# Kernel tuning notes

Measured on AMD Instinct MI355X. Metric: run time of the kernel, lower is better.

Reference implementation:

```python
import jax, jax.numpy as jnp
from jax import lax
import numpy as np

NPOINT, K, EPS = 2048, 16, 1e-5


def fps(xyz, npoint):
    # Farthest point sampling. Deterministic start index 0 (torch uses randint).
    B, N, _ = xyz.shape
    def step(carry, _):
        distance, far = carry
        centroid = jnp.take_along_axis(xyz, far[:, None, None], axis=1)  # [B,1,3]
        d = jnp.sum((xyz - centroid) ** 2, axis=-1)                      # [B,N]
        distance = jnp.minimum(distance, d)
        return (distance, jnp.argmax(distance, axis=-1)), far
    init = (jnp.full((B, N), 1e10, dtype=xyz.dtype), jnp.zeros((B,), jnp.int32))
    _, cent = lax.scan(step, init, None, length=npoint)  # [npoint, B]
    return jnp.transpose(cent)  # [B, npoint]


def gather(points, idx):
    # points [B,N,C], idx [B,...] -> [B,...,C]
    return jax.vmap(lambda p, i: p[i])(points, idx)


def bn_relu(x, gamma, beta):
    # x [B,S,K,C]; BatchNorm2d training-mode stats over (B,S,K) per channel
    mu = jnp.mean(x, axis=(0, 1, 2), keepdims=True)
    var = jnp.var(x, axis=(0, 1, 2), keepdims=True)
    return jax.nn.relu((x - mu) * lax.rsqrt(var + EPS) * gamma + beta)


def setup_inputs() -> dict:
    key = jax.random.key(0)
    ks = jax.random.split(key, 8)
    B, N, C_in, C_out = 4, 8192, 64, 128
    return {
        'xyz': jax.random.normal(ks[0], (B, N, 3), jnp.float32),
        'feat': jax.random.normal(ks[1], (B, N, C_in), jnp.float32),
        'W1': jax.random.normal(ks[2], (C_in + 3, C_out), jnp.float32) * 0.05,
        'g1': jnp.ones((C_out,), jnp.float32),
        'b1': jnp.zeros((C_out,), jnp.float32),
        'W2': jax.random.normal(ks[3], (C_out, C_out), jnp.float32) * 0.05,
        'g2': jnp.ones((C_out,), jnp.float32),
        'b2': jnp.zeros((C_out,), jnp.float32),
    }


def reference(xyz, feat, W1, g1, b1, W2, g2, b2):
    fps_idx = fps(xyz, NPOINT)
    new_xyz = gather(xyz, fps_idx)                              # [B,S,3]
    # squared distances [B,S,N] via ||a||^2 + ||b||^2 - 2 a.b (avoids [B,S,N,3])
    d = (jnp.sum(new_xyz ** 2, -1)[:, :, None]
         + jnp.sum(xyz ** 2, -1)[:, None, :]
         - 2.0 * jnp.einsum('bsc,bnc->bsn', new_xyz, xyz))
    _, idx = lax.top_k(-d, K)                                   # [B,S,K] smallest dists
    g_xyz = gather(xyz, idx)                                    # [B,S,K,3]
    g_feat = gather(feat, idx)                                  # [B,S,K,C]
    x = jnp.concatenate([g_feat, g_xyz - new_xyz[:, :, None]], axis=-1)
    x = bn_relu(jnp.einsum('bskc,co->bsko', x, W1), g1, b1)     # 1x1 conv == matmul
    x = bn_relu(jnp.einsum('bskc,co->bsko', x, W2), g2, b2)
    new_feat = jnp.max(x, axis=2)                               # max over K -> [B,S,Cout]
    return new_xyz, new_feat
```

## Files before the change

kernel.cpp:

```cpp
#include <hip/hip_runtime.h>
#include <hip/hip_bf16.h>

#define N_PTS 8192
#define N_SAMP 2048
#define KNN_K 16
#define NBATCH 4
#define BN_M (NBATCH * N_SAMP * KNN_K)
#define NROWS (N_SAMP * NBATCH * KNN_K)

typedef float f32x2 __attribute__((ext_vector_type(2)));

template <int CTRL, int RM>
__device__ __forceinline__ unsigned umax_dpp(unsigned v) {
  unsigned o = (unsigned)__builtin_amdgcn_update_dpp((int)v, (int)v, CTRL, RM, 0xF, false);
  return (o > v) ? o : v;
}

__global__ __launch_bounds__(512) void fps_kernel(const float* __restrict__ xyz,
                                                  int* __restrict__ fps_idx,
                                                  float* __restrict__ new_xyz) {
#pragma clang fp contract(off)
  __shared__ __align__(16) float xyzw[N_PTS * 4];
  __shared__ int samp[N_SAMP];
  __shared__ unsigned redbuf[8];
  __shared__ unsigned winslot[2];
  const int b = blockIdx.x;
  const int tid = threadIdx.x;
  const int lane = tid & 63;
  const int wid = tid >> 6;
  const float* base = xyz + (size_t)b * N_PTS * 3;
  for (int i = tid; i < N_PTS * 3; i += 512) {
    float v = base[i];
    int p = i / 3, c = i - p * 3;
    xyzw[p * 4 + c] = v;
  }
  for (int i = tid; i < N_PTS; i += 512) xyzw[i * 4 + 3] = 0.f;
  if (tid == 0) { winslot[0] = 0u; winslot[1] = 0xFFFFFFFFu; }
  __syncthreads();

  f32x2 px[8], py[8], pz[8], dmin[8];
#pragma unroll
  for (int j = 0; j < 8; ++j) {
    int p0 = (2 * j) * 512 + tid, p1 = p0 + 512;
    const float4 a = *reinterpret_cast<const float4*>(&xyzw[p0 * 4]);
    const float4 c = *reinterpret_cast<const float4*>(&xyzw[p1 * 4]);
    px[j] = f32x2{a.x, c.x};
    py[j] = f32x2{a.y, c.y};
    pz[j] = f32x2{a.z, c.z};
    dmin[j] = f32x2{1e10f, 1e10f};
  }
  for (int it = 1; it < N_SAMP; ++it) {
    const int p = it & 1;
    const unsigned cur = winslot[p ^ 1];
    if (tid == 0) samp[it - 1] = (int)cur;
    const float4 c4 = *reinterpret_cast<const float4*>(&xyzw[cur * 4]);
    f32x2 cX = {c4.x, c4.x}, cY = {c4.y, c4.y}, cZ = {c4.z, c4.z};
#pragma unroll
    for (int j = 0; j < 8; ++j) {
      f32x2 dx = px[j] - cX;
      f32x2 dy = py[j] - cY;
      f32x2 dz = pz[j] - cZ;
      f32x2 s01 = dx * dx + dy * dy;
      f32x2 d = s01 + dz * dz;
      dmin[j].x = fminf(dmin[j].x, d.x);
      dmin[j].y = fminf(dmin[j].y, d.y);
    }
    f32x2 m0 = {fmaxf(dmin[0].x, dmin[1].x), fmaxf(dmin[0].y, dmin[1].y)};
    f32x2 m1 = {fmaxf(dmin[2].x, dmin[3].x), fmaxf(dmin[2].y, dmin[3].y)};
    f32x2 m2 = {fmaxf(dmin[4].x, dmin[5].x), fmaxf(dmin[4].y, dmin[5].y)};
    f32x2 m3 = {fmaxf(dmin[6].x, dmin[7].x), fmaxf(dmin[6].y, dmin[7].y)};
    f32x2 n0 = {fmaxf(m0.x, m1.x), fmaxf(m0.y, m1.y)};
    f32x2 n1 = {fmaxf(m2.x, m3.x), fmaxf(m2.y, m3.y)};
    f32x2 nn = {fmaxf(n0.x, n1.x), fmaxf(n0.y, n1.y)};
    const unsigned bd = __float_as_uint(fmaxf(nn.x, nn.y));
    unsigned r = bd;
    r = umax_dpp<0xB1, 0xF>(r);
    r = umax_dpp<0x4E, 0xF>(r);
    r = umax_dpp<0x124, 0xF>(r);
    r = umax_dpp<0x128, 0xF>(r);
    r = umax_dpp<0x142, 0xA>(r);
    r = umax_dpp<0x143, 0xC>(r);
    if (lane == 63) redbuf[wid] = r;
    __syncthreads();
    if (tid == 0) winslot[p ^ 1] = 0xFFFFFFFFu;
    unsigned g = redbuf[lane & 7];
    g = umax_dpp<0xB1, 0xF>(g);
    g = umax_dpp<0x4E, 0xF>(g);
    g = umax_dpp<0x124, 0xF>(g);
    if (bd == g) {
      unsigned cand = 0xFFFFFFFFu;
#pragma unroll
      for (int j = 7; j >= 0; --j) {
        if (__float_as_uint(dmin[j].y) == g) cand = (unsigned)((2 * j + 1) * 512 + tid);
        if (__float_as_uint(dmin[j].x) == g) cand = (unsigned)((2 * j) * 512 + tid);
      }
      atomicMin(&winslot[p], cand);
    }
    __syncthreads();
  }
  if (tid == 0) samp[N_SAMP - 1] = (int)winslot[(N_SAMP - 1) & 1];
  __syncthreads();
  for (int s = tid; s < N_SAMP; s += 512) {
    int idx = samp[s];
    fps_idx[b * N_SAMP + s] = idx;
    size_t o = ((size_t)b * N_SAMP + s) * 3;
    new_xyz[o] = xyzw[idx * 4 + 0];
    new_xyz[o + 1] = xyzw[idx * 4 + 1];
    new_xyz[o + 2] = xyzw[idx * 4 + 2];
  }
}

__global__ __launch_bounds__(256) void knn_kernel(const float* __restrict__ xyz,
                                                  const float* __restrict__ new_xyz,
                                                  int* __restrict__ knn_idx) {
  const int wid = threadIdx.x >> 6, lane = threadIdx.x & 63;
  const int q = blockIdx.x * 4 + wid;
  const int b = q >> 11;
  const float* qp = new_xyz + (size_t)q * 3;
  float q0 = qp[0], q1 = qp[1], q2 = qp[2];
  float qn = __fadd_rn(__fadd_rn(__fmul_rn(q0, q0), __fmul_rn(q1, q1)), __fmul_rn(q2, q2));
  const float* pb = xyz + (size_t)b * N_PTS * 3;
  unsigned long long arr[16];
#pragma unroll
  for (int i = 0; i < 16; ++i) arr[i] = ~0ull;
  for (int p = lane; p < N_PTS; p += 64) {
    float p0 = pb[p * 3 + 0], p1 = pb[p * 3 + 1], p2 = pb[p * 3 + 2];
    float pn = __fadd_rn(__fadd_rn(__fmul_rn(p0, p0), __fmul_rn(p1, p1)), __fmul_rn(p2, p2));
    float dt = fmaf(q2, p2, fmaf(q1, p1, __fmul_rn(q0, p0)));
    float d = __fsub_rn(__fadd_rn(qn, pn), __fmul_rn(2.0f, dt));
    unsigned ub = __float_as_uint(d);
    ub ^= (unsigned)((int)ub >> 31) | 0x80000000u;
    unsigned long long key = ((unsigned long long)ub << 32) | (unsigned)p;
    if (key < arr[15]) {
      unsigned long long curk = key;
#pragma unroll
      for (int j = 0; j < 16; ++j) {
        unsigned long long lo = (curk < arr[j]) ? curk : arr[j];
        unsigned long long hi = (curk < arr[j]) ? arr[j] : curk;
        arr[j] = lo; curk = hi;
      }
    }
  }
  for (int r = 0; r < KNN_K; ++r) {
    unsigned long long m = arr[0];
#pragma unroll
    for (int o = 32; o > 0; o >>= 1) {
      unsigned long long other = __shfl_xor(m, o, 64);
      m = (other < m) ? other : m;
    }
    if (arr[0] == m) {
#pragma unroll
      for (int j = 0; j < 15; ++j) arr[j] = arr[j + 1];
      arr[15] = ~0ull;
    }
    if (lane == r) knn_idx[(size_t)q * KNN_K + r] = (int)(m & 0xFFFFFFFFu);
  }
}

__global__ __launch_bounds__(256) void gemm1_kernel(
    const float* __restrict__ xyz, const float* __restrict__ feat,
    const float* __restrict__ W1, const float* __restrict__ new_xyz,
    const int* __restrict__ knn_i, float* __restrict__ y1, float* __restrict__ stats1) {
  __shared__ __align__(16) float At[67 * 128];
  __shared__ __align__(16) float Wq[17 * 128];
  __shared__ float part[4 * 256];
  __shared__ int nb[128];
  const int t = threadIdx.x, blk = blockIdx.x;
  const int row0 = blk * 128;
  if (t < 128) nb[t] = knn_i[row0 + t];
  __syncthreads();
  {
    const int r = t >> 1, q = t & 1;
    const int rg = row0 + r, bs = rg >> 4, b = bs >> 11;
    const float* fr = feat + ((size_t)b * N_PTS + nb[r]) * 64 + q * 32;
#pragma unroll
    for (int i = 0; i < 8; ++i) {
      float4 v = *reinterpret_cast<const float4*>(fr + 4 * i);
      int c = q * 32 + 4 * i;
      At[(c + 0) * 128 + r] = v.x; At[(c + 1) * 128 + r] = v.y;
      At[(c + 2) * 128 + r] = v.z; At[(c + 3) * 128 + r] = v.w;
    }
    if (q == 0) {
      const float* pr = xyz + ((size_t)b * N_PTS + nb[r]) * 3;
      const float* qr = new_xyz + (size_t)bs * 3;
      At[64 * 128 + r] = pr[0] - qr[0];
      At[65 * 128 + r] = pr[1] - qr[1];
      At[66 * 128 + r] = pr[2] - qr[2];
    }
  }
  float acc[8][8];
#pragma unroll
  for (int i = 0; i < 8; ++i)
#pragma unroll
    for (int j = 0; j < 8; ++j) acc[i][j] = 0.f;
  const int ry = t >> 4, cx = t & 15;
  for (int kq = 0; kq < 4; ++kq) {
    const int kbase = kq * 17;
    const int nk = (67 - kbase) < 17 ? (67 - kbase) : 17;
    __syncthreads();
    for (int i = t; i < nk * 32; i += 256)
      reinterpret_cast<float4*>(Wq)[i] =
          reinterpret_cast<const float4*>(W1 + (size_t)kbase * 128)[i];
    __syncthreads();
    for (int kk = 0; kk < nk; ++kk) {
      const float4 a0 = *reinterpret_cast<const float4*>(&At[(kbase + kk) * 128 + ry * 8]);
      const float4 a1 = *reinterpret_cast<const float4*>(&At[(kbase + kk) * 128 + ry * 8 + 4]);
      const float4 w0 = *reinterpret_cast<const float4*>(&Wq[kk * 128 + cx * 8]);
      const float4 w1 = *reinterpret_cast<const float4*>(&Wq[kk * 128 + cx * 8 + 4]);
      const float a[8] = {a0.x, a0.y, a0.z, a0.w, a1.x, a1.y, a1.z, a1.w};
      const float w[8] = {w0.x, w0.y, w0.z, w0.w, w1.x, w1.y, w1.z, w1.w};
#pragma unroll
      for (int i = 0; i < 8; ++i)
#pragma unroll
        for (int j = 0; j < 8; ++j) acc[i][j] = fmaf(a[i], w[j], acc[i][j]);
    }
  }
#pragma unroll
  for (int i = 0; i < 8; ++i) {
    float4 v0 = {acc[i][0], acc[i][1], acc[i][2], acc[i][3]};
    float4 v1 = {acc[i][4], acc[i][5], acc[i][6], acc[i][7]};
    float* dst = y1 + ((size_t)row0 + ry * 8 + i) * 128 + cx * 8;
    *reinterpret_cast<float4*>(dst) = v0;
    *reinterpret_cast<float4*>(dst + 4) = v1;
  }
  float s8[8], q8[8];
#pragma unroll
  for (int j = 0; j < 8; ++j) {
    s8[j] = 0.f; q8[j] = 0.f;
#pragma unroll
    for (int i = 0; i < 8; ++i) { s8[j] += acc[i][j]; q8[j] += acc[i][j] * acc[i][j]; }
  }
#pragma unroll
  for (int j = 0; j < 8; ++j) {
    s8[j] += __shfl_xor(s8[j], 16, 64); q8[j] += __shfl_xor(q8[j], 16, 64);
    s8[j] += __shfl_xor(s8[j], 32, 64); q8[j] += __shfl_xor(q8[j], 32, 64);
  }
  const int w = t >> 6, lane = t & 63;
  if (lane < 16) {
#pragma unroll
    for (int j = 0; j < 8; ++j) {
      part[w * 256 + lane * 8 + j] = s8[j];
      part[w * 256 + 128 + lane * 8 + j] = q8[j];
    }
  }
  __syncthreads();
  {
    int ch = t & 127, which = t >> 7;
    float v = part[0 * 256 + which * 128 + ch] + part[1 * 256 + which * 128 + ch] +
              part[2 * 256 + which * 128 + ch] + part[3 * 256 + which * 128 + ch];
    atomicAdd(&stats1[which * 128 + ch], v);
  }
}

__global__ __launch_bounds__(256) void gemm2_kernel(
    const float* __restrict__ y1, const float* __restrict__ W2,
    const float* __restrict__ stats1, const float* __restrict__ g1v,
    const float* __restrict__ b1v, float* __restrict__ y2, float* __restrict__ stats2) {
  __shared__ __align__(16) float Ah[64 * 128];
  __shared__ __align__(16) float Wq[32 * 128];
  __shared__ float part[4 * 256];
  __shared__ float s1[128], h1[128];
  const int t = threadIdx.x, blk = blockIdx.x;
  const int row0 = blk * 128;
  const float inv_m = 1.0f / (float)BN_M;
  if (t < 128) {
    float m = stats1[t] * inv_m;
    float var = stats1[128 + t] * inv_m - m * m;
    float rs = rsqrtf(var + 1e-5f);
    float sc = rs * g1v[t];
    s1[t] = sc;
    h1[t] = b1v[t] - m * sc;
  }
  float acc[8][8];
#pragma unroll
  for (int i = 0; i < 8; ++i)
#pragma unroll
    for (int j = 0; j < 8; ++j) acc[i][j] = 0.f;
  const int ry = t >> 4, cx = t & 15;
  for (int kh = 0; kh < 2; ++kh) {
    __syncthreads();
    {
      const int r = t >> 1, q = t & 1;
      const float* src = y1 + ((size_t)row0 + r) * 128 + kh * 64 + q * 32;
#pragma unroll
      for (int i = 0; i < 8; ++i) {
        float4 v = *reinterpret_cast<const float4*>(src + 4 * i);
        int c = kh * 64 + q * 32 + 4 * i;
        int cl = c - kh * 64;
        Ah[(cl + 0) * 128 + r] = fmaxf(fmaf(v.x, s1[c + 0], h1[c + 0]), 0.f);
        Ah[(cl + 1) * 128 + r] = fmaxf(fmaf(v.y, s1[c + 1], h1[c + 1]), 0.f);
        Ah[(cl + 2) * 128 + r] = fmaxf(fmaf(v.z, s1[c + 2], h1[c + 2]), 0.f);
        Ah[(cl + 3) * 128 + r] = fmaxf(fmaf(v.w, s1[c + 3], h1[c + 3]), 0.f);
      }
    }
    for (int kq = 0; kq < 2; ++kq) {
      __syncthreads();
      const int kbase = kh * 64 + kq * 32;
      for (int i = t; i < 32 * 32; i += 256)
        reinterpret_cast<float4*>(Wq)[i] =
            reinterpret_cast<const float4*>(W2 + (size_t)kbase * 128)[i];
      __syncthreads();
      for (int kk = 0; kk < 32; ++kk) {
        const int kl = kq * 32 + kk;
        const float4 a0 = *reinterpret_cast<const float4*>(&Ah[kl * 128 + ry * 8]);
        const float4 a1 = *reinterpret_cast<const float4*>(&Ah[kl * 128 + ry * 8 + 4]);
        const float4 w0 = *reinterpret_cast<const float4*>(&Wq[kk * 128 + cx * 8]);
        const float4 w1 = *reinterpret_cast<const float4*>(&Wq[kk * 128 + cx * 8 + 4]);
        const float a[8] = {a0.x, a0.y, a0.z, a0.w, a1.x, a1.y, a1.z, a1.w};
        const float w[8] = {w0.x, w0.y, w0.z, w0.w, w1.x, w1.y, w1.z, w1.w};
#pragma unroll
        for (int i = 0; i < 8; ++i)
#pragma unroll
          for (int j = 0; j < 8; ++j) acc[i][j] = fmaf(a[i], w[j], acc[i][j]);
      }
    }
  }
#pragma unroll
  for (int i = 0; i < 8; ++i) {
    float4 v0 = {acc[i][0], acc[i][1], acc[i][2], acc[i][3]};
    float4 v1 = {acc[i][4], acc[i][5], acc[i][6], acc[i][7]};
    float* dst = y2 + ((size_t)row0 + ry * 8 + i) * 128 + cx * 8;
    *reinterpret_cast<float4*>(dst) = v0;
    *reinterpret_cast<float4*>(dst + 4) = v1;
  }
  float s8[8], q8[8];
#pragma unroll
  for (int j = 0; j < 8; ++j) {
    s8[j] = 0.f; q8[j] = 0.f;
#pragma unroll
    for (int i = 0; i < 8; ++i) { s8[j] += acc[i][j]; q8[j] += acc[i][j] * acc[i][j]; }
  }
#pragma unroll
  for (int j = 0; j < 8; ++j) {
    s8[j] += __shfl_xor(s8[j], 16, 64); q8[j] += __shfl_xor(q8[j], 16, 64);
    s8[j] += __shfl_xor(s8[j], 32, 64); q8[j] += __shfl_xor(q8[j], 32, 64);
  }
  const int w = t >> 6, lane = t & 63;
  if (lane < 16) {
#pragma unroll
    for (int j = 0; j < 8; ++j) {
      part[w * 256 + lane * 8 + j] = s8[j];
      part[w * 256 + 128 + lane * 8 + j] = q8[j];
    }
  }
  __syncthreads();
  {
    int ch = t & 127, which = t >> 7;
    float v = part[0 * 256 + which * 128 + ch] + part[1 * 256 + which * 128 + ch] +
              part[2 * 256 + which * 128 + ch] + part[3 * 256 + which * 128 + ch];
    atomicAdd(&stats2[which * 128 + ch], v);
  }
}

__global__ __launch_bounds__(256) void pool_kernel(
    const float* __restrict__ y2, const float* __restrict__ stats2,
    const float* __restrict__ g2v, const float* __restrict__ b2v,
    float* __restrict__ out_feat) {
  __shared__ float s2[128], h2[128];
  __shared__ float part[4 * 128];
  const int t = threadIdx.x, blk = blockIdx.x;
  const float inv_m = 1.0f / (float)BN_M;
  if (t < 128) {
    float m = stats2[t] * inv_m;
    float var = stats2[128 + t] * inv_m - m * m;
    float rs = rsqrtf(var + 1e-5f);
    float sc = rs * g2v[t];
    s2[t] = sc;
    h2[t] = b2v[t] - m * sc;
  }
  __syncthreads();
  const int c4 = (t & 31) * 4, rg = t >> 5;
  const int lane = t & 63, w = t >> 6;
  for (int s = 0; s < 8; ++s) {
    const int bs = blk * 8 + s;
    float4 m4 = {-1e30f, -1e30f, -1e30f, -1e30f};
#pragma unroll
    for (int rr = 0; rr < 2; ++rr) {
      const int r = bs * 16 + rg * 2 + rr;
      float4 v = *reinterpret_cast<const float4*>(y2 + (size_t)r * 128 + c4);
      float4 z = {fmaxf(fmaf(v.x, s2[c4 + 0], h2[c4 + 0]), 0.f),
                  fmaxf(fmaf(v.y, s2[c4 + 1], h2[c4 + 1]), 0.f),
                  fmaxf(fmaf(v.z, s2[c4 + 2], h2[c4 + 2]), 0.f),
                  fmaxf(fmaf(v.w, s2[c4 + 3], h2[c4 + 3]), 0.f)};
      m4.x = fmaxf(m4.x, z.x); m4.y = fmaxf(m4.y, z.y);
      m4.z = fmaxf(m4.z, z.z); m4.w = fmaxf(m4.w, z.w);
    }
    m4.x = fmaxf(m4.x, __shfl_xor(m4.x, 32, 64));
    m4.y = fmaxf(m4.y, __shfl_xor(m4.y, 32, 64));
    m4.z = fmaxf(m4.z, __shfl_xor(m4.z, 32, 64));
    m4.w = fmaxf(m4.w, __shfl_xor(m4.w, 32, 64));
    if (lane < 32) {
      part[w * 128 + c4 + 0] = m4.x; part[w * 128 + c4 + 1] = m4.y;
      part[w * 128 + c4 + 2] = m4.z; part[w * 128 + c4 + 3] = m4.w;
    }
    __syncthreads();
    if (t < 128) {
      float mm = fmaxf(fmaxf(part[t], part[128 + t]), fmaxf(part[256 + t], part[384 + t]));
      out_feat[(size_t)bs * 128 + t] = mm;
    }
    __syncthreads();
  }
}

extern "C" void kernel_launch(void* const* d_in, const int* in_sizes, int n_in,
                              void* d_out, int out_size, void* d_ws, size_t ws_size,
                              hipStream_t stream) {
  const float* xyz  = (const float*)d_in[0];
  const float* feat = (const float*)d_in[1];
  const float* W1   = (const float*)d_in[2];
  const float* g1   = (const float*)d_in[3];
  const float* b1   = (const float*)d_in[4];
  const float* W2   = (const float*)d_in[5];
  const float* g2   = (const float*)d_in[6];
  const float* b2   = (const float*)d_in[7];
  float* out = (float*)d_out;
  float* new_xyz = out;
  float* out_feat = out + NBATCH * N_SAMP * 3;

  int* fps_i = (int*)d_ws;
  int* knn_i = fps_i + NBATCH * N_SAMP;
  float* stats1 = (float*)(knn_i + NROWS);
  float* stats2 = stats1 + 256;
  float* y1 = stats2 + 256;
  float* y2 = y1 + (size_t)NROWS * 128;

  hipMemsetAsync(stats1, 0, 512 * sizeof(float), stream);
  hipLaunchKernelGGL(fps_kernel, dim3(NBATCH), dim3(512), 0, stream, xyz, fps_i, new_xyz);
  hipLaunchKernelGGL(knn_kernel, dim3((NBATCH * N_SAMP) / 4), dim3(256), 0, stream,
                     xyz, new_xyz, knn_i);
  hipLaunchKernelGGL(gemm1_kernel, dim3(NROWS / 128), dim3(256), 0, stream,
                     xyz, feat, W1, new_xyz, knn_i, y1, stats1);
  hipLaunchKernelGGL(gemm2_kernel, dim3(NROWS / 128), dim3(256), 0, stream,
                     y1, W2, stats1, g1, b1, y2, stats2);
  hipLaunchKernelGGL(pool_kernel, dim3(NBATCH * N_SAMP / 8), dim3(256), 0, stream,
                     y2, stats2, g2, b2, out_feat);
}
```

Measured before the change: 2.233 ms.

## Fuse FPS and KNN into one persistent kernel with progress-flag streaming

Merges farthest-point sampling and KNN into a single launch. Four blocks run FPS and publish sampled coordinates plus a release-ordered progress counter every 32 iterations. The remaining blocks spin on that counter and compute KNN for samples as soon as they are ready. The goal is to hide KNN time behind the serial FPS loop and remove one launch. In exchange, every block reserves the large static LDS array, which limits occupancy to one block per CU, and correctness depends on all blocks being co-resident so the spin-waits cannot deadlock.

```diff
diff --git a/kernel.cpp b/kernel.cpp
--- a/kernel.cpp
+++ b/kernel.cpp
@@ -7,6 +7,7 @@
 #define NBATCH 4
 #define BN_M (NBATCH * N_SAMP * KNN_K)
 #define NROWS (N_SAMP * NBATCH * KNN_K)
+#define KNN_WAVES 2016
 
 typedef float f32x2 __attribute__((ext_vector_type(2)));
 
@@ -16,144 +17,148 @@
   return (o > v) ? o : v;
 }
 
-__global__ __launch_bounds__(512) void fps_kernel(const float* __restrict__ xyz,
-                                                  int* __restrict__ fps_idx,
-                                                  float* __restrict__ new_xyz) {
+__global__ __launch_bounds__(512) void fused_fps_knn(
+    const float* __restrict__ xyz, float* __restrict__ new_xyz,
+    int* __restrict__ knn_idx, int* __restrict__ progress) {
 #pragma clang fp contract(off)
   __shared__ __align__(16) float xyzw[N_PTS * 4];
-  __shared__ int samp[N_SAMP];
   __shared__ unsigned redbuf[8];
   __shared__ unsigned winslot[2];
-  const int b = blockIdx.x;
   const int tid = threadIdx.x;
   const int lane = tid & 63;
-  const int wid = tid >> 6;
-  const float* base = xyz + (size_t)b * N_PTS * 3;
-  for (int i = tid; i < N_PTS * 3; i += 512) {
-    float v = base[i];
-    int p = i / 3, c = i - p * 3;
-    xyzw[p * 4 + c] = v;
-  }
-  for (int i = tid; i < N_PTS; i += 512) xyzw[i * 4 + 3] = 0.f;
-  if (tid == 0) { winslot[0] = 0u; winslot[1] = 0xFFFFFFFFu; }
-  __syncthreads();
-
-  f32x2 px[8], py[8], pz[8], dmin[8];
-#pragma unroll
-  for (int j = 0; j < 8; ++j) {
-    int p0 = (2 * j) * 512 + tid, p1 = p0 + 512;
-    const float4 a = *reinterpret_cast<const float4*>(&xyzw[p0 * 4]);
-    const float4 c = *reinterpret_cast<const float4*>(&xyzw[p1 * 4]);
-    px[j] = f32x2{a.x, c.x};
-    py[j] = f32x2{a.y, c.y};
-    pz[j] = f32x2{a.z, c.z};
-    dmin[j] = f32x2{1e10f, 1e10f};
-  }
-  for (int it = 1; it < N_SAMP; ++it) {
-    const int p = it & 1;
-    const unsigned cur = winslot[p ^ 1];
-    if (tid == 0) samp[it - 1] = (int)cur;
-    const float4 c4 = *reinterpret_cast<const float4*>(&xyzw[cur * 4]);
-    f32x2 cX = {c4.x, c4.x}, cY = {c4.y, c4.y}, cZ = {c4.z, c4.z};
+
+  if (blockIdx.x < NBATCH) {
+    const int b = blockIdx.x;
+    const int wid = tid >> 6;
+    const float* base = xyz + (size_t)b * N_PTS * 3;
+    for (int i = tid; i < N_PTS * 3; i += 512) {
+      float v = base[i];
+      int p = i / 3, c = i - p * 3;
+      xyzw[p * 4 + c] = v;
+    }
+    for (int i = tid; i < N_PTS; i += 512) xyzw[i * 4 + 3] = 0.f;
+    if (tid == 0) { winslot[0] = 0u; winslot[1] = 0xFFFFFFFFu; }
+    __syncthreads();
+
+    f32x2 px[8], py[8], pz[8], dmin[8];
 #pragma unroll
     for (int j = 0; j < 8; ++j) {
-      f32x2 dx = px[j] - cX;
-      f32x2 dy = py[j] - cY;
-      f32x2 dz = pz[j] - cZ;
-      f32x2 s01 = dx * dx + dy * dy;
-      f32x2 d = s01 + dz * dz;
-      dmin[j].x = fminf(dmin[j].x, d.x);
-      dmin[j].y = fminf(dmin[j].y, d.y);
-    }
-    f32x2 m0 = {fmaxf(dmin[0].x, dmin[1].x), fmaxf(dmin[0].y, dmin[1].y)};
-    f32x2 m1 = {fmaxf(dmin[2].x, dmin[3].x), fmaxf(dmin[2].y, dmin[3].y)};
-    f32x2 m2 = {fmaxf(dmin[4].x, dmin[5].x), fmaxf(dmin[4].y, dmin[5].y)};
-    f32x2 m3 = {fmaxf(dmin[6].x, dmin[7].x), fmaxf(dmin[6].y, dmin[7].y)};
-    f32x2 n0 = {fmaxf(m0.x, m1.x), fmaxf(m0.y, m1.y)};
-    f32x2 n1 = {fmaxf(m2.x, m3.x), fmaxf(m2.y, m3.y)};
-    f32x2 nn = {fmaxf(n0.x, n1.x), fmaxf(n0.y, n1.y)};
-    const unsigned bd = __float_as_uint(fmaxf(nn.x, nn.y));
-    unsigned r = bd;
-    r = umax_dpp<0xB1, 0xF>(r);
-    r = umax_dpp<0x4E, 0xF>(r);
-    r = umax_dpp<0x124, 0xF>(r);
-    r = umax_dpp<0x128, 0xF>(r);
-    r = umax_dpp<0x142, 0xA>(r);
-    r = umax_dpp<0x143, 0xC>(r);
-    if (lane == 63) redbuf[wid] = r;
-    __syncthreads();
-    if (tid == 0) winslot[p ^ 1] = 0xFFFFFFFFu;
-    unsigned g = redbuf[lane & 7];
-    g = umax_dpp<0xB1, 0xF>(g);
-    g = umax_dpp<0x4E, 0xF>(g);
-    g = umax_dpp<0x124, 0xF>(g);
-    if (bd == g) {
-      unsigned cand = 0xFFFFFFFFu;
-#pragma unroll
-      for (int j = 7; j >= 0; --j) {
-        if (__float_as_uint(dmin[j].y) == g) cand = (unsigned)((2 * j + 1) * 512 + tid);
-        if (__float_as_uint(dmin[j].x) == g) cand = (unsigned)((2 * j) * 512 + tid);
-      }
-      atomicMin(&winslot[p], cand);
-    }
-    __syncthreads();
-  }
-  if (tid == 0) samp[N_SAMP - 1] = (int)winslot[(N_SAMP - 1) & 1];
-  __syncthreads();
-  for (int s = tid; s < N_SAMP; s += 512) {
-    int idx = samp[s];
-    fps_idx[b * N_SAMP + s] = idx;
-    size_t o = ((size_t)b * N_SAMP + s) * 3;
-    new_xyz[o] = xyzw[idx * 4 + 0];
-    new_xyz[o + 1] = xyzw[idx * 4 + 1];
-    new_xyz[o + 2] = xyzw[idx * 4 + 2];
-  }
-}
-
-__global__ __launch_bounds__(256) void knn_kernel(const float* __restrict__ xyz,
-                                                  const float* __restrict__ new_xyz,
-                                                  int* __restrict__ knn_idx) {
-  const int wid = threadIdx.x >> 6, lane = threadIdx.x & 63;
-  const int q = blockIdx.x * 4 + wid;
-  const int b = q >> 11;
-  const float* qp = new_xyz + (size_t)q * 3;
-  float q0 = qp[0], q1 = qp[1], q2 = qp[2];
-  float qn = __fadd_rn(__fadd_rn(__fmul_rn(q0, q0), __fmul_rn(q1, q1)), __fmul_rn(q2, q2));
-  const float* pb = xyz + (size_t)b * N_PTS * 3;
-  unsigned long long arr[16];
-#pragma unroll
-  for (int i = 0; i < 16; ++i) arr[i] = ~0ull;
-  for (int p = lane; p < N_PTS; p += 64) {
-    float p0 = pb[p * 3 + 0], p1 = pb[p * 3 + 1], p2 = pb[p * 3 + 2];
-    float pn = __fadd_rn(__fadd_rn(__fmul_rn(p0, p0), __fmul_rn(p1, p1)), __fmul_rn(p2, p2));
-    float dt = fmaf(q2, p2, fmaf(q1, p1, __fmul_rn(q0, p0)));
-    float d = __fsub_rn(__fadd_rn(qn, pn), __fmul_rn(2.0f, dt));
-    unsigned ub = __float_as_uint(d);
-    ub ^= (unsigned)((int)ub >> 31) | 0x80000000u;
-    unsigned long long key = ((unsigned long long)ub << 32) | (unsigned)p;
-    if (key < arr[15]) {
-      unsigned long long curk = key;
-#pragma unroll
-      for (int j = 0; j < 16; ++j) {
-        unsigned long long lo = (curk < arr[j]) ? curk : arr[j];
-        unsigned long long hi = (curk < arr[j]) ? arr[j] : curk;
-        arr[j] = lo; curk = hi;
-      }
-    }
-  }
-  for (int r = 0; r < KNN_K; ++r) {
-    unsigned long long m = arr[0];
-#pragma unroll
-    for (int o = 32; o > 0; o >>= 1) {
-      unsigned long long other = __shfl_xor(m, o, 64);
-      m = (other < m) ? other : m;
-    }
-    if (arr[0] == m) {
-#pragma unroll
-      for (int j = 0; j < 15; ++j) arr[j] = arr[j + 1];
-      arr[15] = ~0ull;
-    }
-    if (lane == r) knn_idx[(size_t)q * KNN_K + r] = (int)(m & 0xFFFFFFFFu);
+      int p0 = (2 * j) * 512 + tid, p1 = p0 + 512;
+      const float4 a = *reinterpret_cast<const float4*>(&xyzw[p0 * 4]);
+      const float4 c = *reinterpret_cast<const float4*>(&xyzw[p1 * 4]);
+      px[j] = f32x2{a.x, c.x};
+      py[j] = f32x2{a.y, c.y};
+      pz[j] = f32x2{a.z, c.z};
+      dmin[j] = f32x2{1e10f, 1e10f};
+    }
+    for (int it = 1; it < N_SAMP; ++it) {
+      const int p = it & 1;
+      const unsigned cur = winslot[p ^ 1];
+      const float4 c4 = *reinterpret_cast<const float4*>(&xyzw[cur * 4]);
+      if (tid == 0) {
+        float* dst = new_xyz + ((size_t)b * N_SAMP + (it - 1)) * 3;
+        dst[0] = c4.x; dst[1] = c4.y; dst[2] = c4.z;
+        if ((it & 31) == 0)
+          __hip_atomic_store(&progress[b], it, __ATOMIC_RELEASE, __HIP_MEMORY_SCOPE_AGENT);
+      }
+      f32x2 cX = {c4.x, c4.x}, cY = {c4.y, c4.y}, cZ = {c4.z, c4.z};
+#pragma unroll
+      for (int j = 0; j < 8; ++j) {
+        f32x2 dx = px[j] - cX;
+        f32x2 dy = py[j] - cY;
+        f32x2 dz = pz[j] - cZ;
+        f32x2 s01 = dx * dx + dy * dy;
+        f32x2 d = s01 + dz * dz;
+        dmin[j].x = fminf(dmin[j].x, d.x);
+        dmin[j].y = fminf(dmin[j].y, d.y);
+      }
+      f32x2 m0 = {fmaxf(dmin[0].x, dmin[1].x), fmaxf(dmin[0].y, dmin[1].y)};
+      f32x2 m1 = {fmaxf(dmin[2].x, dmin[3].x), fmaxf(dmin[2].y, dmin[3].y)};
+      f32x2 m2 = {fmaxf(dmin[4].x, dmin[5].x), fmaxf(dmin[4].y, dmin[5].y)};
+      f32x2 m3 = {fmaxf(dmin[6].x, dmin[7].x), fmaxf(dmin[6].y, dmin[7].y)};
+      f32x2 n0 = {fmaxf(m0.x, m1.x), fmaxf(m0.y, m1.y)};
+      f32x2 n1 = {fmaxf(m2.x, m3.x), fmaxf(m2.y, m3.y)};
+      f32x2 nn = {fmaxf(n0.x, n1.x), fmaxf(n0.y, n1.y)};
+      const unsigned bd = __float_as_uint(fmaxf(nn.x, nn.y));
+      unsigned r = bd;
+      r = umax_dpp<0xB1, 0xF>(r);
+      r = umax_dpp<0x4E, 0xF>(r);
+      r = umax_dpp<0x124, 0xF>(r);
+      r = umax_dpp<0x128, 0xF>(r);
+      r = umax_dpp<0x142, 0xA>(r);
+      r = umax_dpp<0x143, 0xC>(r);
+      if (lane == 63) redbuf[wid] = r;
+      __syncthreads();
+      if (tid == 0) winslot[p ^ 1] = 0xFFFFFFFFu;
+      unsigned g = redbuf[lane & 7];
+      g = umax_dpp<0xB1, 0xF>(g);
+      g = umax_dpp<0x4E, 0xF>(g);
+      g = umax_dpp<0x124, 0xF>(g);
+      if (bd == g) {
+        unsigned cand = 0xFFFFFFFFu;
+#pragma unroll
+        for (int j = 7; j >= 0; --j) {
+          if (__float_as_uint(dmin[j].y) == g) cand = (unsigned)((2 * j + 1) * 512 + tid);
+          if (__float_as_uint(dmin[j].x) == g) cand = (unsigned)((2 * j) * 512 + tid);
+        }
+        atomicMin(&winslot[p], cand);
+      }
+      __syncthreads();
+    }
+    if (tid == 0) {
+      unsigned last = winslot[(N_SAMP - 1) & 1];
+      const float4 c4 = *reinterpret_cast<const float4*>(&xyzw[last * 4]);
+      float* dst = new_xyz + ((size_t)b * N_SAMP + (N_SAMP - 1)) * 3;
+      dst[0] = c4.x; dst[1] = c4.y; dst[2] = c4.z;
+      __hip_atomic_store(&progress[b], N_SAMP, __ATOMIC_RELEASE, __HIP_MEMORY_SCOPE_AGENT);
+    }
+  } else {
+    const int wv = (int)(blockIdx.x - NBATCH) * 8 + (tid >> 6);
+    for (int q4 = wv; q4 < NBATCH * N_SAMP; q4 += KNN_WAVES) {
+      const int b = q4 & 3, s = q4 >> 2;
+      while (__hip_atomic_load(&progress[b], __ATOMIC_ACQUIRE, __HIP_MEMORY_SCOPE_AGENT) <= s)
+        __builtin_amdgcn_s_sleep(32);
+      const int q = b * N_SAMP + s;
+      const float* qp = new_xyz + (size_t)q * 3;
+      float q0 = qp[0], q1 = qp[1], q2 = qp[2];
+      float qn = __fadd_rn(__fadd_rn(__fmul_rn(q0, q0), __fmul_rn(q1, q1)), __fmul_rn(q2, q2));
+      const float* pb = xyz + (size_t)b * N_PTS * 3;
+      unsigned long long arr[16];
+#pragma unroll
+      for (int i = 0; i < 16; ++i) arr[i] = ~0ull;
+      for (int p = lane; p < N_PTS; p += 64) {
+        float p0 = pb[p * 3 + 0], p1 = pb[p * 3 + 1], p2 = pb[p * 3 + 2];
+        float pn = __fadd_rn(__fadd_rn(__fmul_rn(p0, p0), __fmul_rn(p1, p1)), __fmul_rn(p2, p2));
+        float dt = fmaf(q2, p2, fmaf(q1, p1, __fmul_rn(q0, p0)));
+        float d = __fsub_rn(__fadd_rn(qn, pn), __fmul_rn(2.0f, dt));
+        unsigned ub = __float_as_uint(d);
+        ub ^= (unsigned)((int)ub >> 31) | 0x80000000u;
+        unsigned long long key = ((unsigned long long)ub << 32) | (unsigned)p;
+        if (key < arr[15]) {
+          unsigned long long curk = key;
+#pragma unroll
+          for (int j = 0; j < 16; ++j) {
+            unsigned long long lo = (curk < arr[j]) ? curk : arr[j];
+            unsigned long long hi = (curk < arr[j]) ? arr[j] : curk;
+            arr[j] = lo; curk = hi;
+          }
+        }
+      }
+      for (int r = 0; r < KNN_K; ++r) {
+        unsigned long long m = arr[0];
+#pragma unroll
+        for (int o = 32; o > 0; o >>= 1) {
+          unsigned long long other = __shfl_xor(m, o, 64);
+          m = (other < m) ? other : m;
+        }
+        if (arr[0] == m) {
+#pragma unroll
+          for (int j = 0; j < 15; ++j) arr[j] = arr[j + 1];
+          arr[15] = ~0ull;
+        }
+        if (lane == r) knn_idx[(size_t)q * KNN_K + r] = (int)(m & 0xFFFFFFFFu);
+      }
+    }
   }
 }
 
@@ -421,13 +426,13 @@
   int* knn_i = fps_i + NBATCH * N_SAMP;
   float* stats1 = (float*)(knn_i + NROWS);
   float* stats2 = stats1 + 256;
-  float* y1 = stats2 + 256;
+  int* progress = (int*)(stats2 + 256);
+  float* y1 = (float*)(progress + 64);
   float* y2 = y1 + (size_t)NROWS * 128;
 
-  hipMemsetAsync(stats1, 0, 512 * sizeof(float), stream);
-  hipLaunchKernelGGL(fps_kernel, dim3(NBATCH), dim3(512), 0, stream, xyz, fps_i, new_xyz);
-  hipLaunchKernelGGL(knn_kernel, dim3((NBATCH * N_SAMP) / 4), dim3(256), 0, stream,
-                     xyz, new_xyz, knn_i);
+  hipMemsetAsync(stats1, 0, (256 + 256 + 64) * sizeof(float), stream);
+  hipLaunchKernelGGL(fused_fps_knn, dim3(NBATCH + 252), dim3(512), 0, stream,
+                     xyz, new_xyz, knn_i, progress);
   hipLaunchKernelGGL(gemm1_kernel, dim3(NROWS / 128), dim3(256), 0, stream,
                      xyz, feat, W1, new_xyz, knn_i, y1, stats1);
   hipLaunchKernelGGL(gemm2_kernel, dim3(NROWS / 128), dim3(256), 0, stream,
```

Result: faster. 2.150 ms (-3.7%).
